# Optimization experiments

Hardware: AMD Instinct MI355X
Metric: run time of the kernel (lower is better)

Reference implementation:

```python
import jax, jax.numpy as jnp
import numpy as np

N = 50000          # nodes
E = 1600000        # edges (avg degree 32)
IN = 9             # raw node feature dim
D = 128            # hidden / out channels
G = 64             # number of graphs in batch
EPS = 1e-5         # LayerNorm eps (torch default)


def _layernorm(h, gamma, beta):
    m = jnp.mean(h, axis=-1, keepdims=True)
    v = jnp.mean((h - m) ** 2, axis=-1, keepdims=True)
    return (h - m) * jax.lax.rsqrt(v + EPS) * gamma + beta


def _sage_conv(h, src, dst, W, b):
    # scatter-mean of neighbor features onto dst, then linear on concat(self, mean)
    nsum = jax.ops.segment_sum(h[src], dst, num_segments=N)            # (N, d)
    cnt = jax.ops.segment_sum(jnp.ones((src.shape[0], 1), h.dtype), dst, num_segments=N)
    nmean = nsum / jnp.maximum(cnt, 1.0)
    return jnp.concatenate([h, nmean], axis=-1) @ W + b               # (N, out)


def setup_inputs() -> dict:
    key = jax.random.key(0)
    ks = jax.random.split(key, 16)
    x = jax.random.normal(ks[0], (N, IN), dtype=jnp.float32)
    edge_index = jax.random.randint(ks[1], (2, E), 0, N, dtype=jnp.int64)
    batch = jnp.sort(jax.random.randint(ks[2], (N,), 0, G, dtype=jnp.int64))

    def lin(k, fin, fout):
        kw, kb = jax.random.split(k)
        s = 1.0 / np.sqrt(fin)
        W = jax.random.uniform(kw, (fin, fout), jnp.float32, -s, s)
        b = jax.random.uniform(kb, (fout,), jnp.float32, -s, s)
        return W, b

    W_emb, b_emb = lin(ks[3], IN, D)
    Wc1, bc1 = lin(ks[4], 2 * D, D)
    Wc2, bc2 = lin(ks[5], 2 * D, D)
    Wc3, bc3 = lin(ks[6], 2 * D, D)
    ones = jnp.ones((D,), jnp.float32)
    zeros = jnp.zeros((D,), jnp.float32)
    return {
        "x": x, "edge_index": edge_index, "batch": batch,
        "W_emb": W_emb, "b_emb": b_emb, "g0": ones, "bt0": zeros,
        "Wc1": Wc1, "bc1": bc1, "g1": ones, "bt1": zeros,
        "Wc2": Wc2, "bc2": bc2, "g2": ones, "bt2": zeros,
        "Wc3": Wc3, "bc3": bc3, "g3": ones, "bt3": zeros,
    }


def reference(x, edge_index, batch, W_emb, b_emb, g0, bt0,
              Wc1, bc1, g1, bt1, Wc2, bc2, g2, bt2, Wc3, bc3, g3, bt3):
    src, dst = edge_index[0], edge_index[1]
    # node embedder: Linear -> LayerNorm -> ReLU
    h = jax.nn.relu(_layernorm(x @ W_emb + b_emb, g0, bt0))
    # 3 SAGE layers (dropout is identity in eval mode)
    h = jax.nn.relu(_layernorm(_sage_conv(h, src, dst, Wc1, bc1), g1, bt1))
    h = jax.nn.relu(_layernorm(_sage_conv(h, src, dst, Wc2, bc2), g2, bt2))
    node_embed = jax.nn.relu(_layernorm(_sage_conv(h, src, dst, Wc3, bc3), g3, bt3))
    # graph pooling: mean + max over nodes per graph
    gsum = jax.ops.segment_sum(node_embed, batch, num_segments=G)
    gcnt = jax.ops.segment_sum(jnp.ones((N, 1), node_embed.dtype), batch, num_segments=G)
    h_mean = gsum / jnp.maximum(gcnt, 1.0)
    h_max = jax.ops.segment_max(node_embed, batch, num_segments=G)  # -inf identity matches torch init
    graph_embed = jnp.concatenate([h_mean, h_max], axis=-1)
    return node_embed, graph_embed
```

## Files before the change

### kernel.cpp

```cpp
#include <hip/hip_runtime.h>
#include <hip/hip_bf16.h>
#include <math.h>

#define NN 50000
#define NNP 50048
#define NE 1600000
#define FIN 9
#define DD 128
#define NG 64
#define PSEG 16
#define LN_EPS 1e-5f

#define NB 196
#define BSHIFT 8
#define CH 8192
#define MAXBE 12288
#define MAXPB 20480

typedef __attribute__((ext_vector_type(8))) short bf16x8;
typedef __attribute__((ext_vector_type(4))) float f32x4;
typedef __attribute__((ext_vector_type(2))) float f32x2;

static __device__ __forceinline__ unsigned short f2b(float f) {
  __hip_bfloat16 h = __float2bfloat16(f);
  return __builtin_bit_cast(unsigned short, h);
}
static __device__ __forceinline__ unsigned char f2e4m3(float f) {
  int r = __builtin_amdgcn_cvt_pk_fp8_f32(f, f, 0, false);
  return (unsigned char)(r & 0xFF);
}

__global__ __launch_bounds__(256) void k_prep(const float* __restrict__ Wc1,
                                              const float* __restrict__ Wc2,
                                              const float* __restrict__ Wc3,
                                              unsigned short* __restrict__ Wt1,
                                              unsigned short* __restrict__ Wt2,
                                              unsigned short* __restrict__ Wt3,
                                              int* __restrict__ bcur,
                                              const int* __restrict__ batch,
                                              int* __restrict__ gstart,
                                              unsigned short* __restrict__ hba,
                                              unsigned short* __restrict__ hbb,
                                              unsigned char* __restrict__ h8,
                                              unsigned int* __restrict__ hmb) {
  const int bid = blockIdx.x;
  const int t = threadIdx.x;
  if (bid < 384) {
    const float* W = (bid < 128) ? Wc1 : (bid < 256) ? Wc2 : Wc3;
    unsigned short* Wt = (bid < 128) ? Wt1 : (bid < 256) ? Wt2 : Wt3;
    int idx = (bid & 127) * 256 + t;
    int k = idx >> 7;
    int n = idx & 127;
    Wt[n * 256 + k] = f2b(W[k * DD + n]);
  } else if (bid == 384) {
    if (t < NB) bcur[t] = t * MAXBE;
    if (t >= 128 && t <= 128 + NG) {
      int g = t - 128;
      int lo = 0, hi = NN;
      while (lo < hi) {
        int mid = (lo + hi) >> 1;
        if (batch[mid] < g) lo = mid + 1; else hi = mid;
      }
      gstart[g] = lo;
    }
  } else if (bid == 385) {
    unsigned int* p = reinterpret_cast<unsigned int*>(hba + (size_t)NN * DD);
    for (int i = t; i < (NNP - NN) * DD / 2; i += 256) p[i] = 0;
  } else if (bid == 386) {
    unsigned int* p = reinterpret_cast<unsigned int*>(hbb + (size_t)NN * DD);
    for (int i = t; i < (NNP - NN) * DD / 2; i += 256) p[i] = 0;
  } else if (bid == 387) {
    unsigned int* p = reinterpret_cast<unsigned int*>(h8 + (size_t)NN * DD);
    for (int i = t; i < (NNP - NN) * DD / 4; i += 256) p[i] = 0;
  } else {
    unsigned int* p = hmb + (size_t)NN * 64;
    for (int i = t; i < (NNP - NN) * 64; i += 256) p[i] = 0;
  }
}

__global__ __launch_bounds__(512) void k_bscatter(const int* __restrict__ src,
                                                  const int* __restrict__ dst,
                                                  int* __restrict__ bcur,
                                                  unsigned int* __restrict__ bents) {
  __shared__ int lh[NB], lbase[NB], gbase[NB], lcnt[NB];
  __shared__ int stmp[256];
  __shared__ unsigned int sbuf[CH];
  const int t = threadIdx.x;
  const int e0 = blockIdx.x * CH;
  const int n = min(CH, NE - e0);

  for (int i = t; i < NB; i += 512) { lh[i] = 0; lcnt[i] = 0; }
  __syncthreads();

  unsigned int ent[16];
  int eb[16];
#pragma unroll
  for (int k = 0; k < 16; ++k) {
    int i = k * 512 + t;
    if (i < n) {
      int s = src[e0 + i], d = dst[e0 + i];
      ent[k] = ((unsigned)d << 16) | (unsigned)s;
      eb[k] = d >> BSHIFT;
      atomicAdd(&lh[eb[k]], 1);
    } else {
      eb[k] = -1;
    }
  }
  __syncthreads();
  if (t < 256) stmp[t] = (t < NB) ? lh[t] : 0;
  __syncthreads();
  for (int off = 1; off < 256; off <<= 1) {
    int v = 0;
    if (t < 256 && t >= off) v = stmp[t - off];
    __syncthreads();
    if (t < 256) stmp[t] += v;
    __syncthreads();
  }
  if (t < NB) lbase[t] = (t == 0) ? 0 : stmp[t - 1];
  __syncthreads();
  if (t < NB && lh[t] > 0) gbase[t] = atomicAdd(&bcur[t], lh[t]);
  __syncthreads();
#pragma unroll
  for (int k = 0; k < 16; ++k) {
    if (eb[k] >= 0) {
      int r = atomicAdd(&lcnt[eb[k]], 1);
      sbuf[lbase[eb[k]] + r] = ent[k];
    }
  }
  __syncthreads();
  for (int i = t; i < n; i += 512) {
    unsigned int e = sbuf[i];
    int b = e >> 24;
    int pos = gbase[b] + (i - lbase[b]);
    if (pos < (b + 1) * MAXBE) bents[pos] = e;
  }
}

__global__ __launch_bounds__(512) void k_sort(const unsigned int* __restrict__ bents,
                                              const int* __restrict__ bcur,
                                              int* __restrict__ prowptr,
                                              int* __restrict__ degv,
                                              unsigned short* __restrict__ csr16) {
  __shared__ int lh[256], lsc[256], plsc[256], lc2[256];
  const int b = blockIdx.x, t = threadIdx.x;
  const int base = b * MAXBE;
  const int nb = min(bcur[b] - base, MAXBE);
  const int pbase = b * MAXPB;

  if (t < 256) { lh[t] = 0; lc2[t] = 0; }
  __syncthreads();
  for (int i = t; i < nb; i += 512)
    atomicAdd(&lh[(bents[base + i] >> 16) & 255], 1);
  __syncthreads();
  if (t < 256) { lsc[t] = lh[t]; plsc[t] = (lh[t] + 31) & ~31; }
  __syncthreads();
  for (int off = 1; off < 256; off <<= 1) {
    int v = 0, pv = 0;
    if (t < 256 && t >= off) { v = lsc[t - off]; pv = plsc[t - off]; }
    __syncthreads();
    if (t < 256) { lsc[t] += v; plsc[t] += pv; }
    __syncthreads();
  }
  int ex = 0, pex = 0;
  if (t < 256) { ex = (t == 0) ? 0 : lsc[t - 1]; pex = (t == 0) ? 0 : plsc[t - 1]; }
  __syncthreads();
  if (t < 256) {
    lsc[t] = ex;
    plsc[t] = pex;
    int gnode = b * 256 + t;
    if (gnode < NN) { prowptr[gnode] = pbase + pex; degv[gnode] = lh[t]; }
  }
  __syncthreads();
  for (int i = t; i < nb; i += 512) {
    unsigned int e = bents[base + i];
    int dl = (e >> 16) & 255;
    int r = atomicAdd(&lc2[dl], 1);
    csr16[pbase + plsc[dl] + r] = (unsigned short)(e & 0xFFFF);
  }
  __syncthreads();
  if (t < 256) {
    int d = lh[t];
    int pd = (d + 31) & ~31;
    int o = pbase + plsc[t];
    for (int k = d; k < pd; ++k) csr16[o + k] = (unsigned short)NN;
  }
}

__global__ __launch_bounds__(256) void k_embed(const float* __restrict__ x,
                                               const float* __restrict__ W,
                                               const float* __restrict__ b,
                                               const float* __restrict__ gamma,
                                               const float* __restrict__ beta,
                                               unsigned short* __restrict__ hout,
                                               unsigned char* __restrict__ h8) {
  const int wid = threadIdx.x >> 6;
  const int lane = threadIdx.x & 63;
  const int node = blockIdx.x * 4 + wid;
  if (node >= NN) return;
  float xr[FIN];
#pragma unroll
  for (int k = 0; k < FIN; ++k) xr[k] = x[node * FIN + k];
  const int c0 = lane, c1 = lane + 64;
  float a0 = b[c0], a1 = b[c1];
#pragma unroll
  for (int k = 0; k < FIN; ++k) {
    a0 += xr[k] * W[k * DD + c0];
    a1 += xr[k] * W[k * DD + c1];
  }
  float s = a0 + a1;
#pragma unroll
  for (int m = 1; m < 64; m <<= 1) s += __shfl_xor(s, m, 64);
  float mean = s * (1.f / DD);
  float d0 = a0 - mean, d1 = a1 - mean;
  float v = d0 * d0 + d1 * d1;
#pragma unroll
  for (int m = 1; m < 64; m <<= 1) v += __shfl_xor(v, m, 64);
  float r = rsqrtf(v * (1.f / DD) + LN_EPS);
  float o0 = fmaxf(d0 * r * gamma[c0] + beta[c0], 0.f);
  float o1 = fmaxf(d1 * r * gamma[c1] + beta[c1], 0.f);
  hout[(size_t)node * DD + c0] = f2b(o0);
  hout[(size_t)node * DD + c1] = f2b(o1);
  h8[(size_t)node * DD + c0] = f2e4m3(o0);
  h8[(size_t)node * DD + c1] = f2e4m3(o1);
}

__global__ __launch_bounds__(256) void k_aggr(const unsigned char* __restrict__ h8,
                                              const int* __restrict__ prowptr,
                                              const int* __restrict__ degv,
                                              const unsigned short* __restrict__ csr16,
                                              unsigned int* __restrict__ hmb) {
  const int wid = __builtin_amdgcn_readfirstlane(threadIdx.x >> 6);
  const int l = threadIdx.x & 63;
  const int node = blockIdx.x * 4 + wid;
  const int pbeg = __builtin_amdgcn_readfirstlane(prowptr[node]);
  const int deg = __builtin_amdgcn_readfirstlane(degv[node]);
  const int nch = (deg + 31) >> 5;
  const unsigned int* __restrict__ cp =
      reinterpret_cast<const unsigned int*>(csr16 + pbeg);
  float a0 = 0.f, a1 = 0.f;
  for (int c = 0; c < nch; ++c) {
#pragma unroll
    for (int q = 0; q < 16; ++q) {
      unsigned int pair = cp[c * 16 + q];
      const unsigned short* r0 =
          reinterpret_cast<const unsigned short*>(h8 + (size_t)(pair & 0xFFFFu) * DD);
      const unsigned short* r1 =
          reinterpret_cast<const unsigned short*>(h8 + (size_t)(pair >> 16) * DD);
      unsigned int u0 = r0[l];
      unsigned int u1 = r1[l];
      f32x2 d0 = __builtin_amdgcn_cvt_pk_f32_fp8((int)u0, false);
      f32x2 d1 = __builtin_amdgcn_cvt_pk_f32_fp8((int)u1, false);
      a0 += d0.x + d1.x;
      a1 += d0.y + d1.y;
    }
  }
  float inv = 1.f / (float)max(deg, 1);
  unsigned int o = ((unsigned int)f2b(a1 * inv) << 16) | (unsigned int)f2b(a0 * inv);
  hmb[(size_t)node * 64 + l] = o;
}

template <int OUT_BF16>
__global__ __launch_bounds__(512, 4) void k_lin_mfma(const unsigned short* __restrict__ hb,
                                                     const unsigned short* __restrict__ hmb,
                                                     const unsigned short* __restrict__ Wt,
                                                     const float* __restrict__ bias,
                                                     const float* __restrict__ gamma,
                                                     const float* __restrict__ beta,
                                                     void* __restrict__ outv,
                                                     unsigned char* __restrict__ h8out) {
  __shared__ unsigned short wlds[128 * 256];
  __shared__ float sred[4][16][2][2];
  const int tid = threadIdx.x;
  const int w = tid >> 6;
  const int l = tid & 63;
  const int g = w & 3;
  const int hh = w >> 2;
  const int c16 = l & 15;
  const int kg = l >> 4;
  const int node = blockIdx.x * 64 + g * 16 + c16;

#pragma unroll
  for (int it = 0; it < 8; ++it) {
    int idx = it * 512 + tid;
    int r = idx >> 5;
    int gr = idx & 31;
    uint4 v = *reinterpret_cast<const uint4*>(Wt + (size_t)r * 256 + gr * 8);
    int gs = gr ^ (r & 7);
    *reinterpret_cast<uint4*>(wlds + (size_t)r * 256 + gs * 8) = v;
  }

  const unsigned short* brow_self = hb + (size_t)node * DD + kg * 8;
  const unsigned short* brow_mean = hmb + (size_t)node * DD + kg * 8;
  bf16x8 bfr[8];
#pragma unroll
  for (int kc = 0; kc < 4; ++kc)
    bfr[kc] = *reinterpret_cast<const bf16x8*>(brow_self + kc * 32);
#pragma unroll
  for (int kc = 0; kc < 4; ++kc)
    bfr[4 + kc] = *reinterpret_cast<const bf16x8*>(brow_mean + kc * 32);

  __syncthreads();

  f32x4 acc[4];
#pragma unroll
  for (int t2 = 0; t2 < 4; ++t2) acc[t2] = (f32x4){0.f, 0.f, 0.f, 0.f};

#pragma unroll
  for (int t2 = 0; t2 < 4; ++t2) {
    const int row = (hh * 4 + t2) * 16 + c16;
    const unsigned short* wr = wlds + (size_t)row * 256;
    const int sw = c16 & 7;
#pragma unroll
    for (int kc = 0; kc < 8; ++kc) {
      bf16x8 a = *reinterpret_cast<const bf16x8*>(wr + ((kc * 4 + kg) ^ sw) * 8);
      acc[t2] = __builtin_amdgcn_mfma_f32_16x16x32_bf16(a, bfr[kc], acc[t2], 0, 0, 0);
    }
  }

#pragma unroll
  for (int t2 = 0; t2 < 4; ++t2) {
    float4 bv = reinterpret_cast<const float4*>(bias)[(hh * 4 + t2) * 4 + kg];
    acc[t2][0] += bv.x; acc[t2][1] += bv.y; acc[t2][2] += bv.z; acc[t2][3] += bv.w;
  }

  float s = 0.f, q = 0.f;
#pragma unroll
  for (int t2 = 0; t2 < 4; ++t2)
#pragma unroll
    for (int i = 0; i < 4; ++i) { float v = acc[t2][i]; s += v; q += v * v; }
#pragma unroll
  for (int m = 16; m < 64; m <<= 1) {
    s += __shfl_xor(s, m, 64);
    q += __shfl_xor(q, m, 64);
  }
  if (kg == 0) { sred[g][c16][hh][0] = s; sred[g][c16][hh][1] = q; }
  __syncthreads();
  float st = sred[g][c16][0][0] + sred[g][c16][1][0];
  float qt = sred[g][c16][0][1] + sred[g][c16][1][1];
  float mean = st * (1.f / DD);
  float var = fmaxf(qt * (1.f / DD) - mean * mean, 0.f);
  float r = rsqrtf(var + LN_EPS);

  if (node < NN) {
#pragma unroll
    for (int t2 = 0; t2 < 4; ++t2) {
      int cbase = (hh * 4 + t2) * 16 + kg * 4;
      float4 gv = reinterpret_cast<const float4*>(gamma)[cbase >> 2];
      float4 btv = reinterpret_cast<const float4*>(beta)[cbase >> 2];
      float v0 = fmaxf((acc[t2][0] - mean) * r * gv.x + btv.x, 0.f);
      float v1 = fmaxf((acc[t2][1] - mean) * r * gv.y + btv.y, 0.f);
      float v2 = fmaxf((acc[t2][2] - mean) * r * gv.z + btv.z, 0.f);
      float v3 = fmaxf((acc[t2][3] - mean) * r * gv.w + btv.w, 0.f);
      if (OUT_BF16) {
        ushort4 ob;
        ob.x = f2b(v0); ob.y = f2b(v1); ob.z = f2b(v2); ob.w = f2b(v3);
        *reinterpret_cast<ushort4*>((unsigned short*)outv + (size_t)node * DD + cbase) = ob;
        int p8 = __builtin_amdgcn_cvt_pk_fp8_f32(v0, v1, 0, false);
        p8 = __builtin_amdgcn_cvt_pk_fp8_f32(v2, v3, p8, true);
        *reinterpret_cast<unsigned int*>(h8out + (size_t)node * DD + cbase) = (unsigned int)p8;
      } else {
        float4 of = make_float4(v0, v1, v2, v3);
        *reinterpret_cast<float4*>((float*)outv + (size_t)node * DD + cbase) = of;
      }
    }
  }
}

__global__ __launch_bounds__(128) void k_pool1(const float* __restrict__ ne,
                                               const int* __restrict__ gstart,
                                               float* __restrict__ part) {
  const int g = blockIdx.x / PSEG;
  const int sg = blockIdx.x % PSEG;
  const int c = threadIdx.x;
  const int beg = gstart[g], end = gstart[g + 1];
  const int len = end - beg;
  const int per = (len + PSEG - 1) / PSEG;
  const int n0 = beg + sg * per;
  const int n1 = min(n0 + per, end);
  float s = 0.f, mx = -INFINITY;
  for (int n = n0; n < n1; ++n) {
    float v = ne[(size_t)n * DD + c];
    s += v;
    mx = fmaxf(mx, v);
  }
  part[(size_t)(g * PSEG + sg) * 256 + c] = s;
  part[(size_t)(g * PSEG + sg) * 256 + 128 + c] = mx;
}

__global__ __launch_bounds__(256) void k_pool2(const float* __restrict__ part,
                                               const int* __restrict__ gstart,
                                               float* __restrict__ gout) {
  const int g = blockIdx.x;
  const int c = threadIdx.x;
  const bool isMax = c >= 128;
  float acc = isMax ? -INFINITY : 0.f;
  for (int sg = 0; sg < PSEG; ++sg) {
    float v = part[(size_t)(g * PSEG + sg) * 256 + c];
    acc = isMax ? fmaxf(acc, v) : (acc + v);
  }
  if (!isMax) acc /= (float)max(gstart[g + 1] - gstart[g], 1);
  gout[(size_t)g * 256 + c] = acc;
}

static inline size_t align_up(size_t v, size_t a) { return (v + a - 1) & ~(a - 1); }

extern "C" void kernel_launch(void* const* d_in, const int* in_sizes, int n_in,
                              void* d_out, int out_size, void* d_ws, size_t ws_size,
                              hipStream_t stream) {
  const float* x     = (const float*)d_in[0];
  const int*   ei    = (const int*)d_in[1];
  const int*   batch = (const int*)d_in[2];
  const float* W_emb = (const float*)d_in[3];
  const float* b_emb = (const float*)d_in[4];
  const float* g0    = (const float*)d_in[5];
  const float* bt0   = (const float*)d_in[6];
  const float* Wc1   = (const float*)d_in[7];
  const float* bc1   = (const float*)d_in[8];
  const float* g1    = (const float*)d_in[9];
  const float* bt1   = (const float*)d_in[10];
  const float* Wc2   = (const float*)d_in[11];
  const float* bc2   = (const float*)d_in[12];
  const float* g2    = (const float*)d_in[13];
  const float* bt2   = (const float*)d_in[14];
  const float* Wc3   = (const float*)d_in[15];
  const float* bc3   = (const float*)d_in[16];
  const float* g3    = (const float*)d_in[17];
  const float* bt3   = (const float*)d_in[18];

  const int* src = ei;
  const int* dst = ei + NE;

  float* out_node  = (float*)d_out;
  float* out_graph = (float*)d_out + (size_t)NN * DD;

  char* p = (char*)d_ws;
  auto alloc = [&](size_t bytes) { char* r = p; p += align_up(bytes, 256); return r; };
  int*            prowptr = (int*)alloc((size_t)NN * sizeof(int));
  int*            degv    = (int*)alloc((size_t)NN * sizeof(int));
  int*            bcur    = (int*)alloc(NB * sizeof(int));
  int*            gstart  = (int*)alloc((NG + 1) * sizeof(int));
  unsigned int*   bents   = (unsigned int*)alloc((size_t)NB * MAXBE * 4);
  unsigned short* csr16   = (unsigned short*)alloc((size_t)NB * MAXPB * 2);
  unsigned short* hba     = (unsigned short*)alloc((size_t)NNP * DD * 2);
  unsigned short* hbb     = (unsigned short*)alloc((size_t)NNP * DD * 2);
  unsigned char*  h8      = (unsigned char*)alloc((size_t)NNP * DD);
  unsigned int*   hmb     = (unsigned int*)alloc((size_t)NNP * 64 * 4);
  unsigned short* Wt1     = (unsigned short*)alloc(128 * 256 * 2);
  unsigned short* Wt2     = (unsigned short*)alloc(128 * 256 * 2);
  unsigned short* Wt3     = (unsigned short*)alloc(128 * 256 * 2);
  float*          ppart   = (float*)alloc((size_t)NG * PSEG * 256 * sizeof(float));

  k_prep<<<388, 256, 0, stream>>>(Wc1, Wc2, Wc3, Wt1, Wt2, Wt3, bcur, batch, gstart,
                                  hba, hbb, h8, hmb);
  k_bscatter<<<(NE + CH - 1) / CH, 512, 0, stream>>>(src, dst, bcur, bents);
  k_sort<<<NB, 512, 0, stream>>>(bents, bcur, prowptr, degv, csr16);

  k_embed<<<NN / 4, 256, 0, stream>>>(x, W_emb, b_emb, g0, bt0, hba, h8);

  const int LIN_GRID = NNP / 64;
  const int AGGR_GRID = NN / 4;
  k_aggr<<<AGGR_GRID, 256, 0, stream>>>(h8, prowptr, degv, csr16, hmb);
  k_lin_mfma<1><<<LIN_GRID, 512, 0, stream>>>(hba, (unsigned short*)hmb, Wt1, bc1, g1, bt1, hbb, h8);
  k_aggr<<<AGGR_GRID, 256, 0, stream>>>(h8, prowptr, degv, csr16, hmb);
  k_lin_mfma<1><<<LIN_GRID, 512, 0, stream>>>(hbb, (unsigned short*)hmb, Wt2, bc2, g2, bt2, hba, h8);
  k_aggr<<<AGGR_GRID, 256, 0, stream>>>(h8, prowptr, degv, csr16, hmb);
  k_lin_mfma<0><<<LIN_GRID, 512, 0, stream>>>(hba, (unsigned short*)hmb, Wt3, bc3, g3, bt3, out_node, h8);

  k_pool1<<<NG * PSEG, 128, 0, stream>>>(out_node, gstart, ppart);
  k_pool2<<<NG, 256, 0, stream>>>(ppart, gstart, out_graph);
}
```

Before: 210.8 us.

## Fuse embed into prep kernel, split-row aggregation, atomic single-pass pooling

```diff
diff --git a/kernel.cpp b/kernel.cpp
--- a/kernel.cpp
+++ b/kernel.cpp
@@ -16,6 +16,7 @@
 #define CH 8192
 #define MAXBE 12288
 #define MAXPB 20480
+#define EMB0 387
 
 typedef __attribute__((ext_vector_type(8))) short bf16x8;
 typedef __attribute__((ext_vector_type(4))) float f32x4;
@@ -42,17 +43,25 @@
                                               unsigned short* __restrict__ hba,
                                               unsigned short* __restrict__ hbb,
                                               unsigned char* __restrict__ h8,
-                                              unsigned int* __restrict__ hmb) {
+                                              unsigned short* __restrict__ hmb,
+                                              float* __restrict__ gout,
+                                              const float* __restrict__ x,
+                                              const float* __restrict__ W,
+                                              const float* __restrict__ b,
+                                              const float* __restrict__ gamma,
+                                              const float* __restrict__ beta) {
   const int bid = blockIdx.x;
   const int t = threadIdx.x;
   if (bid < 384) {
-    const float* W = (bid < 128) ? Wc1 : (bid < 256) ? Wc2 : Wc3;
+    const float* Wc = (bid < 128) ? Wc1 : (bid < 256) ? Wc2 : Wc3;
     unsigned short* Wt = (bid < 128) ? Wt1 : (bid < 256) ? Wt2 : Wt3;
     int idx = (bid & 127) * 256 + t;
     int k = idx >> 7;
     int n = idx & 127;
-    Wt[n * 256 + k] = f2b(W[k * DD + n]);
-  } else if (bid == 384) {
+    Wt[n * 256 + k] = f2b(Wc[k * DD + n]);
+    return;
+  }
+  if (bid == 384) {
     if (t < NB) bcur[t] = t * MAXBE;
     if (t >= 128 && t <= 128 + NG) {
       int g = t - 128;
@@ -63,19 +72,51 @@
       }
       gstart[g] = lo;
     }
-  } else if (bid == 385) {
-    unsigned int* p = reinterpret_cast<unsigned int*>(hba + (size_t)NN * DD);
-    for (int i = t; i < (NNP - NN) * DD / 2; i += 256) p[i] = 0;
-  } else if (bid == 386) {
-    unsigned int* p = reinterpret_cast<unsigned int*>(hbb + (size_t)NN * DD);
-    for (int i = t; i < (NNP - NN) * DD / 2; i += 256) p[i] = 0;
-  } else if (bid == 387) {
-    unsigned int* p = reinterpret_cast<unsigned int*>(h8 + (size_t)NN * DD);
-    for (int i = t; i < (NNP - NN) * DD / 4; i += 256) p[i] = 0;
-  } else {
-    unsigned int* p = hmb + (size_t)NN * 64;
-    for (int i = t; i < (NNP - NN) * 64; i += 256) p[i] = 0;
-  }
+    return;
+  }
+  if (bid == 385) {
+    unsigned int* pa = reinterpret_cast<unsigned int*>(hba + (size_t)NN * DD);
+    unsigned int* pb = reinterpret_cast<unsigned int*>(hbb + (size_t)NN * DD);
+    unsigned int* pm = reinterpret_cast<unsigned int*>(hmb + (size_t)NN * DD);
+    unsigned int* p8 = reinterpret_cast<unsigned int*>(h8 + (size_t)NN * DD);
+    const int n2 = (NNP - NN) * DD / 2;
+    for (int i = t; i < n2; i += 256) { pa[i] = 0; pb[i] = 0; pm[i] = 0; }
+    for (int i = t; i < (NNP - NN) * DD / 4; i += 256) p8[i] = 0;
+    return;
+  }
+  if (bid == 386) {
+    for (int i = t; i < NG * 256; i += 256) gout[i] = 0.f;
+    return;
+  }
+  const int wid = t >> 6;
+  const int lane = t & 63;
+  const int node = (bid - EMB0) * 4 + wid;
+  if (node >= NN) return;
+  float xr[FIN];
+#pragma unroll
+  for (int k = 0; k < FIN; ++k) xr[k] = x[node * FIN + k];
+  const int c0 = lane, c1 = lane + 64;
+  float a0 = b[c0], a1 = b[c1];
+#pragma unroll
+  for (int k = 0; k < FIN; ++k) {
+    a0 += xr[k] * W[k * DD + c0];
+    a1 += xr[k] * W[k * DD + c1];
+  }
+  float s = a0 + a1;
+#pragma unroll
+  for (int m = 1; m < 64; m <<= 1) s += __shfl_xor(s, m, 64);
+  float mean = s * (1.f / DD);
+  float d0 = a0 - mean, d1 = a1 - mean;
+  float v = d0 * d0 + d1 * d1;
+#pragma unroll
+  for (int m = 1; m < 64; m <<= 1) v += __shfl_xor(v, m, 64);
+  float r = rsqrtf(v * (1.f / DD) + LN_EPS);
+  float o0 = fmaxf(d0 * r * gamma[c0] + beta[c0], 0.f);
+  float o1 = fmaxf(d1 * r * gamma[c1] + beta[c1], 0.f);
+  hba[(size_t)node * DD + c0] = f2b(o0);
+  hba[(size_t)node * DD + c1] = f2b(o1);
+  h8[(size_t)node * DD + c0] = f2e4m3(o0);
+  h8[(size_t)node * DD + c1] = f2e4m3(o1);
 }
 
 __global__ __launch_bounds__(512) void k_bscatter(const int* __restrict__ src,
@@ -186,77 +227,46 @@
   }
 }
 
-__global__ __launch_bounds__(256) void k_embed(const float* __restrict__ x,
-                                               const float* __restrict__ W,
-                                               const float* __restrict__ b,
-                                               const float* __restrict__ gamma,
-                                               const float* __restrict__ beta,
-                                               unsigned short* __restrict__ hout,
-                                               unsigned char* __restrict__ h8) {
-  const int wid = threadIdx.x >> 6;
-  const int lane = threadIdx.x & 63;
-  const int node = blockIdx.x * 4 + wid;
-  if (node >= NN) return;
-  float xr[FIN];
-#pragma unroll
-  for (int k = 0; k < FIN; ++k) xr[k] = x[node * FIN + k];
-  const int c0 = lane, c1 = lane + 64;
-  float a0 = b[c0], a1 = b[c1];
-#pragma unroll
-  for (int k = 0; k < FIN; ++k) {
-    a0 += xr[k] * W[k * DD + c0];
-    a1 += xr[k] * W[k * DD + c1];
-  }
-  float s = a0 + a1;
-#pragma unroll
-  for (int m = 1; m < 64; m <<= 1) s += __shfl_xor(s, m, 64);
-  float mean = s * (1.f / DD);
-  float d0 = a0 - mean, d1 = a1 - mean;
-  float v = d0 * d0 + d1 * d1;
-#pragma unroll
-  for (int m = 1; m < 64; m <<= 1) v += __shfl_xor(v, m, 64);
-  float r = rsqrtf(v * (1.f / DD) + LN_EPS);
-  float o0 = fmaxf(d0 * r * gamma[c0] + beta[c0], 0.f);
-  float o1 = fmaxf(d1 * r * gamma[c1] + beta[c1], 0.f);
-  hout[(size_t)node * DD + c0] = f2b(o0);
-  hout[(size_t)node * DD + c1] = f2b(o1);
-  h8[(size_t)node * DD + c0] = f2e4m3(o0);
-  h8[(size_t)node * DD + c1] = f2e4m3(o1);
-}
-
 __global__ __launch_bounds__(256) void k_aggr(const unsigned char* __restrict__ h8,
                                               const int* __restrict__ prowptr,
                                               const int* __restrict__ degv,
                                               const unsigned short* __restrict__ csr16,
-                                              unsigned int* __restrict__ hmb) {
+                                              unsigned short* __restrict__ hmb) {
   const int wid = __builtin_amdgcn_readfirstlane(threadIdx.x >> 6);
   const int l = threadIdx.x & 63;
+  const int lh = l & 31;
+  const int hi = l >> 5;
   const int node = blockIdx.x * 4 + wid;
   const int pbeg = __builtin_amdgcn_readfirstlane(prowptr[node]);
   const int deg = __builtin_amdgcn_readfirstlane(degv[node]);
   const int nch = (deg + 31) >> 5;
   const unsigned int* __restrict__ cp =
       reinterpret_cast<const unsigned int*>(csr16 + pbeg);
-  float a0 = 0.f, a1 = 0.f;
+  float a0 = 0.f, a1 = 0.f, a2 = 0.f, a3 = 0.f;
   for (int c = 0; c < nch; ++c) {
 #pragma unroll
     for (int q = 0; q < 16; ++q) {
       unsigned int pair = cp[c * 16 + q];
-      const unsigned short* r0 =
-          reinterpret_cast<const unsigned short*>(h8 + (size_t)(pair & 0xFFFFu) * DD);
-      const unsigned short* r1 =
-          reinterpret_cast<const unsigned short*>(h8 + (size_t)(pair >> 16) * DD);
-      unsigned int u0 = r0[l];
-      unsigned int u1 = r1[l];
-      f32x2 d0 = __builtin_amdgcn_cvt_pk_f32_fp8((int)u0, false);
-      f32x2 d1 = __builtin_amdgcn_cvt_pk_f32_fp8((int)u1, false);
-      a0 += d0.x + d1.x;
-      a1 += d0.y + d1.y;
-    }
-  }
-  float inv = 1.f / (float)max(deg, 1);
-  unsigned int o = ((unsigned int)f2b(a1 * inv) << 16) | (unsigned int)f2b(a0 * inv);
-  hmb[(size_t)node * 64 + l] = o;
+      int row = hi ? (int)(pair >> 16) : (int)(pair & 0xFFFFu);
+      const unsigned int* rp =
+          reinterpret_cast<const unsigned int*>(h8 + (size_t)row * DD);
+      unsigned int u = rp[lh];
+      f32x2 dlo = __builtin_amdgcn_cvt_pk_f32_fp8((int)u, false);
+      f32x2 dhi = __builtin_amdgcn_cvt_pk_f32_fp8((int)u, true);
+      a0 += dlo.x; a1 += dlo.y; a2 += dhi.x; a3 += dhi.y;
+    }
+  }
+  a0 += __shfl_xor(a0, 32, 64);
+  a1 += __shfl_xor(a1, 32, 64);
+  a2 += __shfl_xor(a2, 32, 64);
+  a3 += __shfl_xor(a3, 32, 64);
+  if (hi == 0) {
+    float inv = 1.f / (float)max(deg, 1);
+    ushort4 o;
+    o.x = f2b(a0 * inv); o.y = f2b(a1 * inv);
+    o.z = f2b(a2 * inv); o.w = f2b(a3 * inv);
+    reinterpret_cast<ushort4*>(hmb + (size_t)node * DD)[lh] = o;
+  }
 }
 
 template <int OUT_BF16>
@@ -366,9 +376,9 @@
   }
 }
 
-__global__ __launch_bounds__(128) void k_pool1(const float* __restrict__ ne,
-                                               const int* __restrict__ gstart,
-                                               float* __restrict__ part) {
+__global__ __launch_bounds__(128) void k_pool(const float* __restrict__ ne,
+                                              const int* __restrict__ gstart,
+                                              float* __restrict__ gout) {
   const int g = blockIdx.x / PSEG;
   const int sg = blockIdx.x % PSEG;
   const int c = threadIdx.x;
@@ -377,29 +387,14 @@
   const int per = (len + PSEG - 1) / PSEG;
   const int n0 = beg + sg * per;
   const int n1 = min(n0 + per, end);
-  float s = 0.f, mx = -INFINITY;
+  float s = 0.f, mx = 0.f;
   for (int n = n0; n < n1; ++n) {
     float v = ne[(size_t)n * DD + c];
     s += v;
     mx = fmaxf(mx, v);
   }
-  part[(size_t)(g * PSEG + sg) * 256 + c] = s;
-  part[(size_t)(g * PSEG + sg) * 256 + 128 + c] = mx;
-}
-
-__global__ __launch_bounds__(256) void k_pool2(const float* __restrict__ part,
-                                               const int* __restrict__ gstart,
-                                               float* __restrict__ gout) {
-  const int g = blockIdx.x;
-  const int c = threadIdx.x;
-  const bool isMax = c >= 128;
-  float acc = isMax ? -INFINITY : 0.f;
-  for (int sg = 0; sg < PSEG; ++sg) {
-    float v = part[(size_t)(g * PSEG + sg) * 256 + c];
-    acc = isMax ? fmaxf(acc, v) : (acc + v);
-  }
-  if (!isMax) acc /= (float)max(gstart[g + 1] - gstart[g], 1);
-  gout[(size_t)g * 256 + c] = acc;
+  atomicAdd(&gout[(size_t)g * 256 + c], s / (float)max(len, 1));
+  atomicMax(reinterpret_cast<int*>(&gout[(size_t)g * 256 + 128 + c]), __float_as_int(mx));
 }
 
 static inline size_t align_up(size_t v, size_t a) { return (v + a - 1) & ~(a - 1); }
@@ -444,28 +439,25 @@
   unsigned short* hba     = (unsigned short*)alloc((size_t)NNP * DD * 2);
   unsigned short* hbb     = (unsigned short*)alloc((size_t)NNP * DD * 2);
   unsigned char*  h8      = (unsigned char*)alloc((size_t)NNP * DD);
-  unsigned int*   hmb     = (unsigned int*)alloc((size_t)NNP * 64 * 4);
+  unsigned short* hmb     = (unsigned short*)alloc((size_t)NNP * DD * 2);
   unsigned short* Wt1     = (unsigned short*)alloc(128 * 256 * 2);
   unsigned short* Wt2     = (unsigned short*)alloc(128 * 256 * 2);
   unsigned short* Wt3     = (unsigned short*)alloc(128 * 256 * 2);
-  float*          ppart   = (float*)alloc((size_t)NG * PSEG * 256 * sizeof(float));
-
-  k_prep<<<388, 256, 0, stream>>>(Wc1, Wc2, Wc3, Wt1, Wt2, Wt3, bcur, batch, gstart,
-                                  hba, hbb, h8, hmb);
+
+  k_prep<<<EMB0 + NN / 4, 256, 0, stream>>>(Wc1, Wc2, Wc3, Wt1, Wt2, Wt3, bcur, batch,
+                                            gstart, hba, hbb, h8, hmb, out_graph,
+                                            x, W_emb, b_emb, g0, bt0);
   k_bscatter<<<(NE + CH - 1) / CH, 512, 0, stream>>>(src, dst, bcur, bents);
   k_sort<<<NB, 512, 0, stream>>>(bents, bcur, prowptr, degv, csr16);
-
-  k_embed<<<NN / 4, 256, 0, stream>>>(x, W_emb, b_emb, g0, bt0, hba, h8);
 
   const int LIN_GRID = NNP / 64;
   const int AGGR_GRID = NN / 4;
   k_aggr<<<AGGR_GRID, 256, 0, stream>>>(h8, prowptr, degv, csr16, hmb);
-  k_lin_mfma<1><<<LIN_GRID, 512, 0, stream>>>(hba, (unsigned short*)hmb, Wt1, bc1, g1, bt1, hbb, h8);
+  k_lin_mfma<1><<<LIN_GRID, 512, 0, stream>>>(hba, hmb, Wt1, bc1, g1, bt1, hbb, h8);
   k_aggr<<<AGGR_GRID, 256, 0, stream>>>(h8, prowptr, degv, csr16, hmb);
-  k_lin_mfma<1><<<LIN_GRID, 512, 0, stream>>>(hbb, (unsigned short*)hmb, Wt2, bc2, g2, bt2, hba, h8);
+  k_lin_mfma<1><<<LIN_GRID, 512, 0, stream>>>(hbb, hmb, Wt2, bc2, g2, bt2, hba, h8);
   k_aggr<<<AGGR_GRID, 256, 0, stream>>>(h8, prowptr, degv, csr16, hmb);
-  k_lin_mfma<0><<<LIN_GRID, 512, 0, stream>>>(hba, (unsigned short*)hmb, Wt3, bc3, g3, bt3, out_node, h8);
-
-  k_pool1<<<NG * PSEG, 128, 0, stream>>>(out_node, gstart, ppart);
-  k_pool2<<<NG, 256, 0, stream>>>(ppart, gstart, out_graph);
-}
+  k_lin_mfma<0><<<LIN_GRID, 512, 0, stream>>>(hba, hmb, Wt3, bc3, g3, bt3, out_node, h8);
+
+  k_pool<<<NG * PSEG, 128, 0, stream>>>(out_node, gstart, out_graph);
+}
```

Result: faster. 206.6 us (median of 2 runs) (-2.0%).
